# Kernel optimization log

Hardware: AMD Instinct MI355X
Metric: run time of the kernel (lower is better)

The kernel has to match this reference:

```python
import jax, jax.numpy as jnp
import numpy as np

S, LC = 4096, 16
N_WORD, N_CHAR = 100000, 128
CHAR_DIM, CHAR_HIDDEN = 64, 128
N_DIM, N_HIDDEN, N_TAG = 256, 512, 64


def setup_inputs() -> dict:
    key = jax.random.key(0)
    ks = jax.random.split(key, 16)
    rn = lambda k, shape, s=0.1: (jax.random.normal(k, shape, jnp.float32) * s)
    inp = {
        'char_emb': rn(ks[0], (N_CHAR, CHAR_DIM), 1.0),
        'char_Wih': rn(ks[1], (4 * CHAR_HIDDEN, CHAR_DIM)),
        'char_Whh': rn(ks[2], (4 * CHAR_HIDDEN, CHAR_HIDDEN)),
        'char_bih': rn(ks[3], (4 * CHAR_HIDDEN,)),
        'char_bhh': rn(ks[4], (4 * CHAR_HIDDEN,)),
        'word_emb': rn(ks[5], (N_WORD, N_DIM), 1.0),
        'Wih': rn(ks[6], (4 * N_HIDDEN, N_DIM + CHAR_HIDDEN)),
        'Whh': rn(ks[7], (4 * N_HIDDEN, N_HIDDEN)),
        'bih': rn(ks[8], (4 * N_HIDDEN,)),
        'bhh': rn(ks[9], (4 * N_HIDDEN,)),
        'W1': rn(ks[10], (N_TAG, N_HIDDEN)),
        'b1': rn(ks[11], (N_TAG,)),
        'x': jax.random.randint(ks[12], (S,), 0, N_WORD),
        'chars': jax.random.randint(ks[13], (S, LC), 0, N_CHAR),
        'char_lens': jax.random.randint(ks[14], (S,), 1, LC + 1),
    }
    return inp


def _lstm(xs, mask, Wih, Whh, bih, bhh):
    # xs: [T, B, In], mask: [T, B] bool. PyTorch gate order: i, f, g, o.
    T, B, _ = xs.shape
    H = Whh.shape[1]
    def step(carry, inp):
        h, c = carry
        x_t, m_t = inp
        g = x_t @ Wih.T + bih + h @ Whh.T + bhh  # [B, 4H]
        i, f, gg, o = jnp.split(g, 4, axis=-1)
        c_new = jax.nn.sigmoid(f) * c + jax.nn.sigmoid(i) * jnp.tanh(gg)
        h_new = jax.nn.sigmoid(o) * jnp.tanh(c_new)
        m = m_t[:, None]
        h2 = jnp.where(m, h_new, h)
        c2 = jnp.where(m, c_new, c)
        return (h2, c2), h2
    init = (jnp.zeros((B, H), xs.dtype), jnp.zeros((B, H), xs.dtype))
    (h_fin, _), hs = jax.lax.scan(step, init, (xs, mask))
    return hs, h_fin


def reference(char_emb, char_Wih, char_Whh, char_bih, char_bhh,
              word_emb, Wih, Whh, bih, bhh, W1, b1,
              x, chars, char_lens):
    # --- char-level LSTM, all S words batched (replaces per-word Python loop) ---
    cx = char_emb[chars]                      # [S, LC, char_dim]
    cx = jnp.transpose(cx, (1, 0, 2))         # [LC, S, char_dim]
    cmask = jnp.arange(LC)[:, None] < char_lens[None, :]  # [LC, S]
    _, char_h = _lstm(cx, cmask, char_Wih, char_Whh, char_bih, char_bhh)  # [S, char_hidden]

    # --- word-level LSTM over the sentence (batch 1, as in original) ---
    wx = word_emb[x]                          # [S, n_dim]
    feat = jnp.concatenate([wx, char_h], axis=-1)[:, None, :]  # [S, 1, n_dim+char_hidden]
    wmask = jnp.ones((feat.shape[0], 1), bool)
    hs, _ = _lstm(feat, wmask, Wih, Whh, bih, bhh)  # [S, 1, n_hidden]
    hs = hs[:, 0, :]

    logits = hs @ W1.T + b1                   # [S, n_tag]
    return jax.nn.log_softmax(logits, axis=-1)
```

## Files before the change

### kernel.cpp

```cpp
#include <hip/hip_runtime.h>
#include <hip/hip_bf16.h>


#define OFF_FLAG  0
#define OFF_CEMB  16
#define OFF_CWIH  8208
#define OFF_CBIH  40976
#define OFF_CBHH  41488
#define OFF_CWHH  42000
#define OFF_BIH   107536
#define OFF_BHH   109584
#define OFF_W1T   111632
#define OFF_CGE   144400
#define OFF_CH    209936
#define OFF_XP2   734224
#define OFF_HH    4928528

#define SENT 0xFFFFFFFFu

__device__ __forceinline__ float sigf(float x) { return 1.0f / (1.0f + __expf(-x)); }
__device__ __forceinline__ float tanh_f(float x) { return 2.0f * sigf(2.0f * x) - 1.0f; }
__device__ __forceinline__ float b2f_lo(unsigned u) { return __uint_as_float(u << 16); }
__device__ __forceinline__ float b2f_hi(unsigned u) { return __uint_as_float(u & 0xFFFF0000u); }
__device__ __forceinline__ float4 dec2(uint2 u) {
    return make_float4(b2f_lo(u.x), b2f_hi(u.x), b2f_lo(u.y), b2f_hi(u.y));
}
__device__ __forceinline__ unsigned f2bf_bits(float f) {
    unsigned b = __float_as_uint(f);
    b += 0x7FFFu + ((b >> 16) & 1u);
    return b >> 16;
}

__global__ void detect_kernel(const unsigned* __restrict__ w, int* __restrict__ flagp) {
    unsigned v = w[threadIdx.x];
    unsigned e = (v >> 7) & 0xFF;
    int inr = (e >= 100 && e <= 140) ? 1 : 0;
    unsigned long long m = __ballot(inr);
    if (threadIdx.x == 0) flagp[0] = (__popcll(m) >= 56) ? 1 : 0;
}

__global__ void convf_kernel(const void* __restrict__ s, float* __restrict__ d,
                             int n, const int* __restrict__ flagp) {
    int i = blockIdx.x * 256 + threadIdx.x;
    if (i >= n) return;
    d[i] = flagp[0] ? __bfloat162float(((const __hip_bfloat16*)s)[i])
                    : ((const float*)s)[i];
}

__global__ void w1t_kernel(const void* __restrict__ W1, float* __restrict__ W1T,
                           const int* __restrict__ flagp) {
    int i = blockIdx.x * 256 + threadIdx.x;
    int j = i & 63, k = i >> 6;
    W1T[i] = flagp[0] ? __bfloat162float(((const __hip_bfloat16*)W1)[j * 512 + k])
                      : ((const float*)W1)[j * 512 + k];
}

__global__ void __launch_bounds__(256) cge_kernel(
    const float* __restrict__ cemb, const float* __restrict__ cWih,
    const float* __restrict__ cbih, const float* __restrict__ cbhh,
    float* __restrict__ cge)
{
    __shared__ float xe[64];
    int c = blockIdx.x, tid = threadIdx.x;
    if (tid < 64) xe[tid] = cemb[c * 64 + tid];
    __syncthreads();
#pragma unroll
    for (int rep = 0; rep < 2; ++rep) {
        int j = rep * 256 + tid;
        float acc = cbih[j] + cbhh[j];
#pragma unroll 8
        for (int k = 0; k < 64; ++k)
            acc += xe[k] * cWih[j * 64 + k];
        cge[c * 512 + j] = acc;
    }
}

__global__ void __launch_bounds__(256) char_lstm_kernel(
    const float* __restrict__ cge, const float* __restrict__ Whh,
    const int* __restrict__ chars, const int* __restrict__ lens,
    float* __restrict__ char_h)
{
    __shared__ float hls[16][128];
    int tid = threadIdx.x;
    int wl = tid >> 4, sl = tid & 15;
    int w = blockIdx.x * 16 + wl;
    int len = lens[w];
    const int* cw = chars + w * 16;
    float c[8];
#pragma unroll
    for (int q = 0; q < 8; ++q) { c[q] = 0.0f; hls[wl][sl * 8 + q] = 0.0f; }

    for (int t = 0; t < 16; ++t) {
        __syncthreads();
        int ch = cw[t];
        const float* xg = cge + ch * 512;
        float acc[4][8];
#pragma unroll
        for (int g = 0; g < 4; ++g)
#pragma unroll
            for (int q = 0; q < 8; ++q)
                acc[g][q] = xg[g * 128 + sl * 8 + q];

        const float4* h4 = (const float4*)hls[wl];
#pragma unroll
        for (int g = 0; g < 4; ++g) {
            const float4* wbase = ((const float4*)Whh) + (g * 128 + sl * 8) * 32;
            for (int k4 = 0; k4 < 32; ++k4) {
                float4 hv = h4[k4];
#pragma unroll
                for (int q = 0; q < 8; ++q) {
                    float4 wv = wbase[q * 32 + k4];
                    acc[g][q] += wv.x * hv.x + wv.y * hv.y + wv.z * hv.z + wv.w * hv.w;
                }
            }
        }
        __syncthreads();
        if (t < len) {
#pragma unroll
            for (int q = 0; q < 8; ++q) {
                float iv = sigf(acc[0][q]);
                float fv = sigf(acc[1][q]);
                float gv = tanh_f(acc[2][q]);
                float ov = sigf(acc[3][q]);
                c[q] = fv * c[q] + iv * gv;
                hls[wl][sl * 8 + q] = ov * tanh_f(c[q]);
            }
        }
    }
    __syncthreads();
#pragma unroll
    for (int q = 0; q < 8; ++q)
        char_h[w * 128 + sl * 8 + q] = hls[wl][sl * 8 + q];
}

__global__ void __launch_bounds__(256) xp2_kernel(
    const void* __restrict__ wemb, const int* __restrict__ x,
    const float* __restrict__ char_h, const void* __restrict__ Wraw,
    const float* __restrict__ bih, const float* __restrict__ bhh,
    __hip_bfloat16* __restrict__ xp2, const int* __restrict__ flagp)
{
    __shared__ float feat[16][384];
    int flag = flagp[0];
    int tid = threadIdx.x, tl = tid >> 4, sl = tid & 15;
    int t = blockIdx.x * 16 + tl;
    int xw = x[t];
    for (int idx = sl; idx < 384; idx += 16) {
        float v;
        if (idx < 256)
            v = flag ? __bfloat162float(((const __hip_bfloat16*)wemb)[(size_t)xw * 256 + idx])
                     : ((const float*)wemb)[(size_t)xw * 256 + idx];
        else
            v = char_h[t * 128 + (idx - 256)];
        feat[tl][idx] = v;
    }
    __syncthreads();

    const float4* f4 = (const float4*)feat[tl];
    for (int rb = 0; rb < 4; ++rb) {
        int r0 = rb * 512 + sl * 32;
        for (int qc = 0; qc < 4; ++qc) {
            int rr = r0 + qc * 8;
            float acc[8];
#pragma unroll
            for (int q = 0; q < 8; ++q)
                acc[q] = bih[rr + q] + bhh[rr + q];
            if (!flag) {
                const float4* wb = ((const float4*)Wraw) + (size_t)rr * 96;
                for (int k4 = 0; k4 < 96; ++k4) {
                    float4 fv = f4[k4];
#pragma unroll
                    for (int q = 0; q < 8; ++q) {
                        float4 wv = wb[q * 96 + k4];
                        acc[q] += wv.x * fv.x + wv.y * fv.y + wv.z * fv.z + wv.w * fv.w;
                    }
                }
            } else {
                const uint2* wb = ((const uint2*)Wraw) + (size_t)rr * 96;
                for (int k4 = 0; k4 < 96; ++k4) {
                    float4 fv = f4[k4];
#pragma unroll
                    for (int q = 0; q < 8; ++q) {
                        uint2 wv = wb[q * 96 + k4];
                        acc[q] += b2f_lo(wv.x) * fv.x + b2f_hi(wv.x) * fv.y
                                + b2f_lo(wv.y) * fv.z + b2f_hi(wv.y) * fv.w;
                    }
                }
            }
#pragma unroll
            for (int q = 0; q < 8; ++q)
                xp2[(size_t)t * 2048 + rr + q] = __float2bfloat16(acc[q]);
        }
    }
}

__global__ void __launch_bounds__(1024, 4) word_lstm_kernel(
    const __hip_bfloat16* __restrict__ xp2, const void* __restrict__ Whh_raw,
    unsigned* __restrict__ hview, const int* __restrict__ flagp)
{
    __shared__ float hbuf[16][576];
    __shared__ float hout[2][32];
    int flag = flagp[0];
    int wg = blockIdx.x;
    int tid = threadIdx.x;
    int wave = tid >> 6, lane = tid & 63;
    int sp = lane >> 5;
    int g  = (lane >> 3) & 3;
    int kk = lane & 7;
    int slot = wg * 32 + wave * 2 + sp;
    int grow = g * 512 + slot;
    int ownidx = ((lane >> 4) == (wg & 3)) ? (wg >> 2) : -1;

    float4 w00, w01, w02, w03, w04, w05, w06, w07;
    float4 w08, w09, w10, w11, w12, w13, w14, w15;
    if (!flag) {
        const float4* wr = (const float4*)((const float*)Whh_raw + (size_t)grow * 512 + kk * 64);
        w00 = wr[0];  w01 = wr[1];  w02 = wr[2];  w03 = wr[3];
        w04 = wr[4];  w05 = wr[5];  w06 = wr[6];  w07 = wr[7];
        w08 = wr[8];  w09 = wr[9];  w10 = wr[10]; w11 = wr[11];
        w12 = wr[12]; w13 = wr[13]; w14 = wr[14]; w15 = wr[15];
    } else {
        const uint2* wr = (const uint2*)((const unsigned short*)Whh_raw + (size_t)grow * 512 + kk * 64);
        w00 = dec2(wr[0]);  w01 = dec2(wr[1]);  w02 = dec2(wr[2]);  w03 = dec2(wr[3]);
        w04 = dec2(wr[4]);  w05 = dec2(wr[5]);  w06 = dec2(wr[6]);  w07 = dec2(wr[7]);
        w08 = dec2(wr[8]);  w09 = dec2(wr[9]);  w10 = dec2(wr[10]); w11 = dec2(wr[11]);
        w12 = dec2(wr[12]); w13 = dec2(wr[13]); w14 = dec2(wr[14]); w15 = dec2(wr[15]);
    }
#define PIN4(a,b,c,d) asm volatile("" : "+v"(a.x),"+v"(a.y),"+v"(a.z),"+v"(a.w), \
    "+v"(b.x),"+v"(b.y),"+v"(b.z),"+v"(b.w), "+v"(c.x),"+v"(c.y),"+v"(c.z),"+v"(c.w), \
    "+v"(d.x),"+v"(d.y),"+v"(d.z),"+v"(d.w))
    PIN4(w00, w01, w02, w03); PIN4(w04, w05, w06, w07);
    PIN4(w08, w09, w10, w11); PIN4(w12, w13, w14, w15);
#undef PIN4

    const unsigned short* xpr = (const unsigned short*)xp2;
    float* wbuf = hbuf[wave];
    float c = 0.0f;
    int dead = 0;

    for (int t = 0; t < 4096; ++t) {
        unsigned short xraw = xpr[(size_t)t * 2048 + grow];

        if (t == 0) {
#pragma unroll
            for (int i = 0; i < 8; ++i)
                wbuf[(2 * i + (lane >> 5)) * 36 + (lane & 31)] = 0.0f;
        } else {
            const unsigned* src = hview + (size_t)(t - 1) * 256;
            const float* houtprev = hout[(t - 1) & 1];
            unsigned v[4];
            unsigned spins = 0;
            for (;;) {
#pragma unroll
                for (int i = 0; i < 4; ++i)
                    v[i] = __hip_atomic_load(src + lane + i * 64, __ATOMIC_RELAXED,
                                             __HIP_MEMORY_SCOPE_AGENT);
                int ok = 1;
#pragma unroll
                for (int i = 0; i < 4; ++i) ok &= (i == ownidx) | (v[i] != SENT);
                if (dead || __all(ok)) break;
                if (++spins > (1u << 22)) { dead = 1; break; }
            }
            if (dead) {
#pragma unroll
                for (int i = 0; i < 4; ++i)
                    if (i != ownidx && v[i] == SENT) v[i] = 0x3f803f80u;
            }
#pragma unroll
            for (int i = 0; i < 4; ++i) {
                int ch = (lane >> 4) + 4 * i;
                float f0, f1;
                if (i == ownidx) {
                    f0 = houtprev[2 * (lane & 15)];
                    f1 = houtprev[2 * (lane & 15) + 1];
                } else {
                    f0 = b2f_lo(v[i]);
                    f1 = b2f_hi(v[i]);
                }
                wbuf[ch * 36 + 2 * (lane & 15)]     = f0;
                wbuf[ch * 36 + 2 * (lane & 15) + 1] = f1;
            }
        }

        const float4* p0 = (const float4*)(wbuf + kk * 72);
        const float4* p1 = (const float4*)(wbuf + kk * 72 + 36);
        float a0 = 0.0f, a1 = 0.0f, a2 = 0.0f, a3 = 0.0f;
        {
            float4 hv;
#define FMA4_(A, W, HV) A += (W).x*(HV).x + (W).y*(HV).y + (W).z*(HV).z + (W).w*(HV).w
            hv = p0[0]; FMA4_(a0, w00, hv);  hv = p0[1]; FMA4_(a1, w01, hv);
            hv = p0[2]; FMA4_(a2, w02, hv);  hv = p0[3]; FMA4_(a3, w03, hv);
            hv = p0[4]; FMA4_(a0, w04, hv);  hv = p0[5]; FMA4_(a1, w05, hv);
            hv = p0[6]; FMA4_(a2, w06, hv);  hv = p0[7]; FMA4_(a3, w07, hv);
            hv = p1[0]; FMA4_(a0, w08, hv);  hv = p1[1]; FMA4_(a1, w09, hv);
            hv = p1[2]; FMA4_(a2, w10, hv);  hv = p1[3]; FMA4_(a3, w11, hv);
            hv = p1[4]; FMA4_(a0, w12, hv);  hv = p1[5]; FMA4_(a1, w13, hv);
            hv = p1[6]; FMA4_(a2, w14, hv);  hv = p1[7]; FMA4_(a3, w15, hv);
#undef FMA4_
        }
        float acc = (a0 + a1) + (a2 + a3);
        acc += __shfl_xor(acc, 1);
        acc += __shfl_xor(acc, 2);
        acc += __shfl_xor(acc, 4);
        float gvt = acc + __bfloat162float(*(const __hip_bfloat16*)&xraw);

        float iv = __shfl(gvt, sp * 32 + 0);
        float fv = __shfl(gvt, sp * 32 + 8);
        float gg = __shfl(gvt, sp * 32 + 16);
        float ov = __shfl(gvt, sp * 32 + 24);
        c = sigf(fv) * c + sigf(iv) * tanh_f(gg);
        float h = sigf(ov) * tanh_f(c);

        if ((lane & 31) == 0) hout[t & 1][wave * 2 + sp] = h;
        __syncthreads();

        if (wave == 0 && lane < 16) {
            unsigned u0 = f2bf_bits(hout[t & 1][2 * lane]);
            unsigned u1 = f2bf_bits(hout[t & 1][2 * lane + 1]);
            __hip_atomic_store(hview + (size_t)t * 256 + wg * 16 + lane,
                               u0 | (u1 << 16),
                               __ATOMIC_RELAXED, __HIP_MEMORY_SCOPE_AGENT);
        }
    }
}

__global__ void __launch_bounds__(64) out_kernel(
    const unsigned short* __restrict__ hh16, const float* __restrict__ W1T,
    const void* __restrict__ b1raw, void* __restrict__ out,
    const int* __restrict__ flagp)
{
    __shared__ float hb[512];
    int flag = flagp[0];
    int t = blockIdx.x, j = threadIdx.x;
    const unsigned* src = (const unsigned*)(hh16 + (size_t)t * 512);
#pragma unroll
    for (int kq = 0; kq < 4; ++kq) {
        unsigned u = src[j * 4 + kq];
        hb[j * 8 + 2 * kq]     = b2f_lo(u);
        hb[j * 8 + 2 * kq + 1] = b2f_hi(u);
    }
    __syncthreads();

    float acc = flag ? __bfloat162float(((const __hip_bfloat16*)b1raw)[j])
                     : ((const float*)b1raw)[j];
#pragma unroll 8
    for (int k = 0; k < 512; ++k)
        acc += hb[k] * W1T[k * 64 + j];

    float m = acc;
#pragma unroll
    for (int o = 32; o; o >>= 1) m = fmaxf(m, __shfl_xor(m, o));
    float e = __expf(acc - m);
    float s = e;
#pragma unroll
    for (int o = 32; o; o >>= 1) s += __shfl_xor(s, o);
    float r = acc - m - __logf(s);
    if (flag) ((__hip_bfloat16*)out)[t * 64 + j] = __float2bfloat16(r);
    else      ((float*)out)[t * 64 + j] = r;
}

extern "C" void kernel_launch(void* const* d_in, const int* in_sizes, int n_in,
                              void* d_out, int out_size, void* d_ws, size_t ws_size,
                              hipStream_t stream)
{
    (void)in_sizes; (void)n_in; (void)out_size; (void)ws_size;
    const void* char_emb = d_in[0];
    const void* char_Wih = d_in[1];
    const void* char_Whh = d_in[2];
    const void* char_bih = d_in[3];
    const void* char_bhh = d_in[4];
    const void* word_emb = d_in[5];
    const void* Wih      = d_in[6];
    const void* Whh      = d_in[7];
    const void* bih      = d_in[8];
    const void* bhh      = d_in[9];
    const void* W1       = d_in[10];
    const void* b1       = d_in[11];
    const int* x     = (const int*)d_in[12];
    const int* chars = (const int*)d_in[13];
    const int* lens  = (const int*)d_in[14];

    float* ws    = (float*)d_ws;
    int*   flagp = (int*)(ws + OFF_FLAG);
    float* cembf = ws + OFF_CEMB;
    float* cWihf = ws + OFF_CWIH;
    float* cbihf = ws + OFF_CBIH;
    float* cbhhf = ws + OFF_CBHH;
    float* cWhhf = ws + OFF_CWHH;
    float* bihf  = ws + OFF_BIH;
    float* bhhf  = ws + OFF_BHH;
    float* W1T   = ws + OFF_W1T;
    float* cge   = ws + OFF_CGE;
    float* charh = ws + OFF_CH;
    __hip_bfloat16* xp2 = (__hip_bfloat16*)(ws + OFF_XP2);
    unsigned short* hh16 = (unsigned short*)(ws + OFF_HH);

    hipMemsetAsync(hh16, 0xFF, (size_t)4096 * 512 * 2, stream);

    detect_kernel<<<1, 64, 0, stream>>>((const unsigned*)char_emb, flagp);

    convf_kernel<<<(8192 + 255) / 256, 256, 0, stream>>>(char_emb, cembf, 8192, flagp);
    convf_kernel<<<(32768 + 255) / 256, 256, 0, stream>>>(char_Wih, cWihf, 32768, flagp);
    convf_kernel<<<2, 256, 0, stream>>>(char_bih, cbihf, 512, flagp);
    convf_kernel<<<2, 256, 0, stream>>>(char_bhh, cbhhf, 512, flagp);
    convf_kernel<<<(65536 + 255) / 256, 256, 0, stream>>>(char_Whh, cWhhf, 65536, flagp);
    convf_kernel<<<8, 256, 0, stream>>>(bih, bihf, 2048, flagp);
    convf_kernel<<<8, 256, 0, stream>>>(bhh, bhhf, 2048, flagp);
    w1t_kernel<<<128, 256, 0, stream>>>(W1, W1T, flagp);

    cge_kernel<<<128, 256, 0, stream>>>(cembf, cWihf, cbihf, cbhhf, cge);
    char_lstm_kernel<<<256, 256, 0, stream>>>(cge, cWhhf, chars, lens, charh);
    xp2_kernel<<<256, 256, 0, stream>>>(word_emb, x, charh, Wih, bihf, bhhf, xp2, flagp);
    word_lstm_kernel<<<16, 1024, 0, stream>>>(xp2, Whh, (unsigned*)hh16, flagp);
    out_kernel<<<4096, 64, 0, stream>>>(hh16, W1T, b1, d_out, flagp);
}
```

Before: 13.85 ms.

## Switch word LSTM recurrence to fp16 weights and hidden state with dot2

Converts Whh to fp16 in a pre-pass and keeps the recurrent weights packed in registers as half2, computing the recurrent matvec with fdot2 instead of fp32 FMAs. The hidden state exchanged between workgroups is now fp16, and each wave copies the packed values straight into smaller LDS buffers without unpacking. The special case that read its own block's h from local memory is dropped, so every block polls all of the global h. This cuts register pressure, LDS traffic and ALU work on the serial critical path, at the cost of fp16 precision and range and one extra conversion kernel.

```diff
diff --git a/kernel.cpp b/kernel.cpp
--- a/kernel.cpp
+++ b/kernel.cpp
@@ -1,5 +1,6 @@
 #include <hip/hip_runtime.h>
 #include <hip/hip_bf16.h>
+#include <hip/hip_fp16.h>
 
 
 #define OFF_FLAG  0
@@ -15,20 +16,47 @@
 #define OFF_CH    209936
 #define OFF_XP2   734224
 #define OFF_HH    4928528
+#define OFF_WHH16 5977104
 
 #define SENT 0xFFFFFFFFu
+
+#ifndef __has_builtin
+#define __has_builtin(x) 0
+#endif
+#if __has_builtin(__builtin_amdgcn_fdot2)
+#define HASDOT2 1
+#endif
+
+typedef _Float16 v2h __attribute__((ext_vector_type(2)));
 
 __device__ __forceinline__ float sigf(float x) { return 1.0f / (1.0f + __expf(-x)); }
 __device__ __forceinline__ float tanh_f(float x) { return 2.0f * sigf(2.0f * x) - 1.0f; }
 __device__ __forceinline__ float b2f_lo(unsigned u) { return __uint_as_float(u << 16); }
 __device__ __forceinline__ float b2f_hi(unsigned u) { return __uint_as_float(u & 0xFFFF0000u); }
-__device__ __forceinline__ float4 dec2(uint2 u) {
-    return make_float4(b2f_lo(u.x), b2f_hi(u.x), b2f_lo(u.y), b2f_hi(u.y));
-}
-__device__ __forceinline__ unsigned f2bf_bits(float f) {
-    unsigned b = __float_as_uint(f);
-    b += 0x7FFFu + ((b >> 16) & 1u);
-    return b >> 16;
+__device__ __forceinline__ float h2f_lo(unsigned u) {
+    union { unsigned short s; _Float16 h; } c;
+    c.s = (unsigned short)(u & 0xFFFFu);
+    return (float)c.h;
+}
+__device__ __forceinline__ float h2f_hi(unsigned u) {
+    union { unsigned short s; _Float16 h; } c;
+    c.s = (unsigned short)(u >> 16);
+    return (float)c.h;
+}
+__device__ __forceinline__ unsigned short f2h_bits(float f) {
+    union { unsigned short s; _Float16 h; } c;
+    c.h = (_Float16)f;
+    return c.s;
+}
+__device__ __forceinline__ float dot2h(unsigned w, unsigned h, float acc) {
+#ifdef HASDOT2
+    union U { unsigned u; v2h v; };
+    U uw; uw.u = w;
+    U uh; uh.u = h;
+    return __builtin_amdgcn_fdot2(uw.v, uh.v, acc, false);
+#else
+    return acc + h2f_lo(w) * h2f_lo(h) + h2f_hi(w) * h2f_hi(h);
+#endif
 }
 
 __global__ void detect_kernel(const unsigned* __restrict__ w, int* __restrict__ flagp) {
@@ -53,6 +81,14 @@
     int j = i & 63, k = i >> 6;
     W1T[i] = flagp[0] ? __bfloat162float(((const __hip_bfloat16*)W1)[j * 512 + k])
                       : ((const float*)W1)[j * 512 + k];
+}
+
+__global__ void whh16_kernel(const void* __restrict__ src, unsigned short* __restrict__ dst,
+                             const int* __restrict__ flagp) {
+    int i = blockIdx.x * 256 + threadIdx.x;
+    float f = flagp[0] ? __bfloat162float(((const __hip_bfloat16*)src)[i])
+                       : ((const float*)src)[i];
+    dst[i] = f2h_bits(f);
 }
 
 __global__ void __launch_bounds__(256) cge_kernel(
@@ -194,12 +230,11 @@
 }
 
 __global__ void __launch_bounds__(1024, 4) word_lstm_kernel(
-    const __hip_bfloat16* __restrict__ xp2, const void* __restrict__ Whh_raw,
-    unsigned* __restrict__ hview, const int* __restrict__ flagp)
-{
-    __shared__ float hbuf[16][576];
+    const __hip_bfloat16* __restrict__ xp2, const unsigned* __restrict__ whh16,
+    unsigned* __restrict__ hview)
+{
+    __shared__ unsigned hbuf[16][320];
     __shared__ float hout[2][32];
-    int flag = flagp[0];
     int wg = blockIdx.x;
     int tid = threadIdx.x;
     int wave = tid >> 6, lane = tid & 63;
@@ -208,95 +243,71 @@
     int kk = lane & 7;
     int slot = wg * 32 + wave * 2 + sp;
     int grow = g * 512 + slot;
-    int ownidx = ((lane >> 4) == (wg & 3)) ? (wg >> 2) : -1;
-
-    float4 w00, w01, w02, w03, w04, w05, w06, w07;
-    float4 w08, w09, w10, w11, w12, w13, w14, w15;
-    if (!flag) {
-        const float4* wr = (const float4*)((const float*)Whh_raw + (size_t)grow * 512 + kk * 64);
-        w00 = wr[0];  w01 = wr[1];  w02 = wr[2];  w03 = wr[3];
-        w04 = wr[4];  w05 = wr[5];  w06 = wr[6];  w07 = wr[7];
-        w08 = wr[8];  w09 = wr[9];  w10 = wr[10]; w11 = wr[11];
-        w12 = wr[12]; w13 = wr[13]; w14 = wr[14]; w15 = wr[15];
-    } else {
-        const uint2* wr = (const uint2*)((const unsigned short*)Whh_raw + (size_t)grow * 512 + kk * 64);
-        w00 = dec2(wr[0]);  w01 = dec2(wr[1]);  w02 = dec2(wr[2]);  w03 = dec2(wr[3]);
-        w04 = dec2(wr[4]);  w05 = dec2(wr[5]);  w06 = dec2(wr[6]);  w07 = dec2(wr[7]);
-        w08 = dec2(wr[8]);  w09 = dec2(wr[9]);  w10 = dec2(wr[10]); w11 = dec2(wr[11]);
-        w12 = dec2(wr[12]); w13 = dec2(wr[13]); w14 = dec2(wr[14]); w15 = dec2(wr[15]);
-    }
-#define PIN4(a,b,c,d) asm volatile("" : "+v"(a.x),"+v"(a.y),"+v"(a.z),"+v"(a.w), \
-    "+v"(b.x),"+v"(b.y),"+v"(b.z),"+v"(b.w), "+v"(c.x),"+v"(c.y),"+v"(c.z),"+v"(c.w), \
-    "+v"(d.x),"+v"(d.y),"+v"(d.z),"+v"(d.w))
-    PIN4(w00, w01, w02, w03); PIN4(w04, w05, w06, w07);
-    PIN4(w08, w09, w10, w11); PIN4(w12, w13, w14, w15);
-#undef PIN4
+
+    const uint4* wr = (const uint4*)(whh16 + (size_t)grow * 256) + kk * 8;
+    uint4 wa0 = wr[0], wa1 = wr[1], wa2 = wr[2], wa3 = wr[3];
+    uint4 wa4 = wr[4], wa5 = wr[5], wa6 = wr[6], wa7 = wr[7];
 
     const unsigned short* xpr = (const unsigned short*)xp2;
-    float* wbuf = hbuf[wave];
+    unsigned* wbuf = hbuf[wave];
     float c = 0.0f;
     int dead = 0;
 
+#define PINU4(a) asm volatile("" : "+v"(a.x), "+v"(a.y), "+v"(a.z), "+v"(a.w))
     for (int t = 0; t < 4096; ++t) {
         unsigned short xraw = xpr[(size_t)t * 2048 + grow];
+        PINU4(wa0); PINU4(wa1); PINU4(wa2); PINU4(wa3);
+        PINU4(wa4); PINU4(wa5); PINU4(wa6); PINU4(wa7);
 
         if (t == 0) {
 #pragma unroll
-            for (int i = 0; i < 8; ++i)
-                wbuf[(2 * i + (lane >> 5)) * 36 + (lane & 31)] = 0.0f;
+            for (int i = 0; i < 4; ++i)
+                wbuf[((lane >> 4) + 4 * i) * 20 + (lane & 15)] = 0u;
         } else {
-            const unsigned* src = hview + (size_t)(t - 1) * 256;
-            const float* houtprev = hout[(t - 1) & 1];
+            const unsigned* src = hview + (size_t)(t - 1) * 256 + lane;
             unsigned v[4];
             unsigned spins = 0;
             for (;;) {
 #pragma unroll
                 for (int i = 0; i < 4; ++i)
-                    v[i] = __hip_atomic_load(src + lane + i * 64, __ATOMIC_RELAXED,
+                    v[i] = __hip_atomic_load(src + i * 64, __ATOMIC_RELAXED,
                                              __HIP_MEMORY_SCOPE_AGENT);
                 int ok = 1;
 #pragma unroll
-                for (int i = 0; i < 4; ++i) ok &= (i == ownidx) | (v[i] != SENT);
+                for (int i = 0; i < 4; ++i) ok &= (v[i] != SENT);
                 if (dead || __all(ok)) break;
                 if (++spins > (1u << 22)) { dead = 1; break; }
             }
             if (dead) {
 #pragma unroll
                 for (int i = 0; i < 4; ++i)
-                    if (i != ownidx && v[i] == SENT) v[i] = 0x3f803f80u;
+                    if (v[i] == SENT) v[i] = 0x3C003C00u;
             }
 #pragma unroll
-            for (int i = 0; i < 4; ++i) {
-                int ch = (lane >> 4) + 4 * i;
-                float f0, f1;
-                if (i == ownidx) {
-                    f0 = houtprev[2 * (lane & 15)];
-                    f1 = houtprev[2 * (lane & 15) + 1];
-                } else {
-                    f0 = b2f_lo(v[i]);
-                    f1 = b2f_hi(v[i]);
-                }
-                wbuf[ch * 36 + 2 * (lane & 15)]     = f0;
-                wbuf[ch * 36 + 2 * (lane & 15) + 1] = f1;
-            }
+            for (int i = 0; i < 4; ++i)
+                wbuf[((lane >> 4) + 4 * i) * 20 + (lane & 15)] = v[i];
         }
 
-        const float4* p0 = (const float4*)(wbuf + kk * 72);
-        const float4* p1 = (const float4*)(wbuf + kk * 72 + 36);
+        const uint4* q0 = (const uint4*)(wbuf + (2 * kk) * 20);
+        const uint4* q1 = (const uint4*)(wbuf + (2 * kk) * 20 + 20);
         float a0 = 0.0f, a1 = 0.0f, a2 = 0.0f, a3 = 0.0f;
-        {
-            float4 hv;
-#define FMA4_(A, W, HV) A += (W).x*(HV).x + (W).y*(HV).y + (W).z*(HV).z + (W).w*(HV).w
-            hv = p0[0]; FMA4_(a0, w00, hv);  hv = p0[1]; FMA4_(a1, w01, hv);
-            hv = p0[2]; FMA4_(a2, w02, hv);  hv = p0[3]; FMA4_(a3, w03, hv);
-            hv = p0[4]; FMA4_(a0, w04, hv);  hv = p0[5]; FMA4_(a1, w05, hv);
-            hv = p0[6]; FMA4_(a2, w06, hv);  hv = p0[7]; FMA4_(a3, w07, hv);
-            hv = p1[0]; FMA4_(a0, w08, hv);  hv = p1[1]; FMA4_(a1, w09, hv);
-            hv = p1[2]; FMA4_(a2, w10, hv);  hv = p1[3]; FMA4_(a3, w11, hv);
-            hv = p1[4]; FMA4_(a0, w12, hv);  hv = p1[5]; FMA4_(a1, w13, hv);
-            hv = p1[6]; FMA4_(a2, w14, hv);  hv = p1[7]; FMA4_(a3, w15, hv);
-#undef FMA4_
-        }
+        uint4 h4;
+        h4 = q0[0]; a0 = dot2h(wa0.x, h4.x, a0); a1 = dot2h(wa0.y, h4.y, a1);
+                    a2 = dot2h(wa0.z, h4.z, a2); a3 = dot2h(wa0.w, h4.w, a3);
+        h4 = q0[1]; a0 = dot2h(wa1.x, h4.x, a0); a1 = dot2h(wa1.y, h4.y, a1);
+                    a2 = dot2h(wa1.z, h4.z, a2); a3 = dot2h(wa1.w, h4.w, a3);
+        h4 = q0[2]; a0 = dot2h(wa2.x, h4.x, a0); a1 = dot2h(wa2.y, h4.y, a1);
+                    a2 = dot2h(wa2.z, h4.z, a2); a3 = dot2h(wa2.w, h4.w, a3);
+        h4 = q0[3]; a0 = dot2h(wa3.x, h4.x, a0); a1 = dot2h(wa3.y, h4.y, a1);
+                    a2 = dot2h(wa3.z, h4.z, a2); a3 = dot2h(wa3.w, h4.w, a3);
+        h4 = q1[0]; a0 = dot2h(wa4.x, h4.x, a0); a1 = dot2h(wa4.y, h4.y, a1);
+                    a2 = dot2h(wa4.z, h4.z, a2); a3 = dot2h(wa4.w, h4.w, a3);
+        h4 = q1[1]; a0 = dot2h(wa5.x, h4.x, a0); a1 = dot2h(wa5.y, h4.y, a1);
+                    a2 = dot2h(wa5.z, h4.z, a2); a3 = dot2h(wa5.w, h4.w, a3);
+        h4 = q1[2]; a0 = dot2h(wa6.x, h4.x, a0); a1 = dot2h(wa6.y, h4.y, a1);
+                    a2 = dot2h(wa6.z, h4.z, a2); a3 = dot2h(wa6.w, h4.w, a3);
+        h4 = q1[3]; a0 = dot2h(wa7.x, h4.x, a0); a1 = dot2h(wa7.y, h4.y, a1);
+                    a2 = dot2h(wa7.z, h4.z, a2); a3 = dot2h(wa7.w, h4.w, a3);
         float acc = (a0 + a1) + (a2 + a3);
         acc += __shfl_xor(acc, 1);
         acc += __shfl_xor(acc, 2);
@@ -314,13 +325,14 @@
         __syncthreads();
 
         if (wave == 0 && lane < 16) {
-            unsigned u0 = f2bf_bits(hout[t & 1][2 * lane]);
-            unsigned u1 = f2bf_bits(hout[t & 1][2 * lane + 1]);
+            unsigned u0 = f2h_bits(hout[t & 1][2 * lane]);
+            unsigned u1 = f2h_bits(hout[t & 1][2 * lane + 1]);
             __hip_atomic_store(hview + (size_t)t * 256 + wg * 16 + lane,
                                u0 | (u1 << 16),
                                __ATOMIC_RELAXED, __HIP_MEMORY_SCOPE_AGENT);
         }
     }
+#undef PINU4
 }
 
 __global__ void __launch_bounds__(64) out_kernel(
@@ -335,8 +347,8 @@
 #pragma unroll
     for (int kq = 0; kq < 4; ++kq) {
         unsigned u = src[j * 4 + kq];
-        hb[j * 8 + 2 * kq]     = b2f_lo(u);
-        hb[j * 8 + 2 * kq + 1] = b2f_hi(u);
+        hb[j * 8 + 2 * kq]     = h2f_lo(u);
+        hb[j * 8 + 2 * kq + 1] = h2f_hi(u);
     }
     __syncthreads();
 
@@ -393,8 +405,9 @@
     float* charh = ws + OFF_CH;
     __hip_bfloat16* xp2 = (__hip_bfloat16*)(ws + OFF_XP2);
     unsigned short* hh16 = (unsigned short*)(ws + OFF_HH);
-
-    hipMemsetAsync(hh16, 0xFF, (size_t)4096 * 512 * 2, stream);
+    unsigned short* whh16 = (unsigned short*)(ws + OFF_WHH16);
+
+    (void)hipMemsetAsync(hh16, 0xFF, (size_t)4096 * 512 * 2, stream);
 
     detect_kernel<<<1, 64, 0, stream>>>((const unsigned*)char_emb, flagp);
 
@@ -406,10 +419,11 @@
     convf_kernel<<<8, 256, 0, stream>>>(bih, bihf, 2048, flagp);
     convf_kernel<<<8, 256, 0, stream>>>(bhh, bhhf, 2048, flagp);
     w1t_kernel<<<128, 256, 0, stream>>>(W1, W1T, flagp);
+    whh16_kernel<<<4096, 256, 0, stream>>>(Whh, whh16, flagp);
 
     cge_kernel<<<128, 256, 0, stream>>>(cembf, cWihf, cbihf, cbhhf, cge);
     char_lstm_kernel<<<256, 256, 0, stream>>>(cge, cWhhf, chars, lens, charh);
     xp2_kernel<<<256, 256, 0, stream>>>(word_emb, x, charh, Wih, bihf, bhhf, xp2, flagp);
-    word_lstm_kernel<<<16, 1024, 0, stream>>>(xp2, Whh, (unsigned*)hh16, flagp);
+    word_lstm_kernel<<<16, 1024, 0, stream>>>(xp2, (const unsigned*)whh16, (unsigned*)hh16);
     out_kernel<<<4096, 64, 0, stream>>>(hh16, W1T, b1, d_out, flagp);
 }
```

After: 13.33 ms. 3.7% less time.
